# Optimization experiments

Measured on AMD Instinct MI355X. Metric: run time of the kernel, lower is better.

The kernel has to match this reference:

```python
import jax, jax.numpy as jnp
import numpy as np

N, E = 50000, 800000
IN, MID, OUT = 128, 256, 128
LN_EPS = 1e-5


def layer_norm(x, gamma, beta, eps=LN_EPS):
    mu = jnp.mean(x, axis=-1, keepdims=True)
    var = jnp.mean(jnp.square(x - mu), axis=-1, keepdims=True)
    return (x - mu) * jax.lax.rsqrt(var + eps) * gamma + beta


def gcn_conv(x, W, b, src, dst, norm, n):
    # x' = D^{-1/2}(A+I)D^{-1/2} X W + b  (self-loops already folded into src/dst/norm)
    h = x @ W                                  # [N, F_out]
    msg = h[src] * norm[:, None]               # [E+N, F_out] gather + scale
    out = jax.ops.segment_sum(msg, dst, num_segments=n)
    return out + b


def setup_inputs() -> dict:
    key = jax.random.key(0)
    ks = jax.random.split(key, 4)
    x = jax.random.normal(ks[0], (N, IN), dtype=jnp.float32)
    edge_index = jax.random.randint(ks[1], (2, E), 0, N, dtype=jnp.int32)
    W1 = jax.random.normal(ks[2], (IN, MID), dtype=jnp.float32) * (1.0 / np.sqrt(IN))
    b1 = jnp.zeros((MID,), jnp.float32)
    g1 = jnp.ones((IN,), jnp.float32)
    be1 = jnp.zeros((IN,), jnp.float32)
    W4 = jax.random.normal(ks[3], (MID, OUT), dtype=jnp.float32) * (1.0 / np.sqrt(MID))
    b4 = jnp.zeros((OUT,), jnp.float32)
    g4 = jnp.ones((MID,), jnp.float32)
    be4 = jnp.zeros((MID,), jnp.float32)
    return {"x": x, "W1": W1, "b1": b1, "g1": g1, "be1": be1,
            "W4": W4, "b4": b4, "g4": g4, "be4": be4,
            "edge_index": edge_index}


def reference(x, W1, b1, g1, be1, W4, b4, g4, be4, edge_index):
    n = x.shape[0]
    loop = jnp.arange(n, dtype=edge_index.dtype)
    src = jnp.concatenate([edge_index[0], loop])   # [E+N]
    dst = jnp.concatenate([edge_index[1], loop])   # [E+N]
    deg = jax.ops.segment_sum(jnp.ones_like(src, x.dtype), dst, num_segments=n)
    dinv = jax.lax.rsqrt(deg)                      # deg >= 1 thanks to self-loops
    norm = dinv[src] * dinv[dst]                   # [E+N]

    h = gcn_conv(layer_norm(x, g1, be1), W1, b1, src, dst, norm, n)
    h = jax.nn.gelu(h, approximate=False)          # torch F.gelu default = exact erf
    h = gcn_conv(layer_norm(h, g4, be4), W4, b4, src, dst, norm, n)
    return h
```

## Files before the change

kernel.cpp:

```cpp
#include <hip/hip_runtime.h>
#include <math.h>

#define N_NODES 50000
#define E_EDGES 800000

typedef __attribute__((ext_vector_type(4))) float f32x4;
typedef __attribute__((ext_vector_type(8))) short s16x8;

#define T1_OFF    0UL
#define A1H_OFF   12800000UL
#define A1L_OFF   25600000UL
#define T2B_OFF   38400000UL
#define WB1H_OFF  64000000UL
#define WB1L_OFF  64100096UL
#define WB4H_OFF  64200192UL
#define WB4L_OFF  64300288UL
#define DINV_OFF  64400384UL
#define HIST8_OFF 64600384UL
#define RP8_OFF   66200384UL
#define POSREL_OFF 67800448UL
#define CSRS_OFF  71000448UL
#define BSUM_OFF  74200448UL

__device__ __forceinline__ float lo16f(unsigned u) { return __uint_as_float(u << 16); }
__device__ __forceinline__ float hi16f(unsigned u) { return __uint_as_float(u & 0xffff0000u); }
__device__ __forceinline__ unsigned pack2bf(float a, float b) {
  unsigned ua = __float_as_uint(a); ua += 0x7fffu + ((ua >> 16) & 1u);
  unsigned ub = __float_as_uint(b); ub += 0x7fffu + ((ub >> 16) & 1u);
  return (ua >> 16) | (ub & 0xffff0000u);
}
__device__ __forceinline__ float gelu_f(float x) {
  return 0.5f * x * (1.f + erff(x * 0.70710678118654752f));
}

__global__ __launch_bounds__(256) void zero_hist8(int4* __restrict__ h) {
  int i = blockIdx.x * 256 + threadIdx.x;
  if (i < 100000) h[i] = make_int4(0, 0, 0, 0);
}

__global__ __launch_bounds__(256) void edge_pos(const int* __restrict__ dst,
                                                int* __restrict__ hist8,
                                                int* __restrict__ posrel) {
  int e = blockIdx.x * 256 + threadIdx.x;
  int d = dst[e];
  int seg = blockIdx.x & 7;
  int r = atomicAdd(&hist8[d * 8 + seg], 1);
  __builtin_nontemporal_store(r, posrel + e);
}

__global__ __launch_bounds__(1024) void scan_partial(const int* __restrict__ hist,
                                                     int* __restrict__ rp,
                                                     int* __restrict__ bsum, int n) {
  __shared__ int wsum[16];
  int tid = threadIdx.x, lane = tid & 63, wv = tid >> 6;
  int i = blockIdx.x * 1024 + tid;
  int v = (i < n) ? hist[i] : 0;
  int sc = v;
  #pragma unroll
  for (int m = 1; m < 64; m <<= 1) { int o = __shfl_up(sc, m); if (lane >= m) sc += o; }
  if (lane == 63) wsum[wv] = sc;
  __syncthreads();
  if (wv == 0) {
    int w = (lane < 16) ? wsum[lane] : 0;
    int swc = w;
    #pragma unroll
    for (int m = 1; m < 16; m <<= 1) { int o = __shfl_up(swc, m); if (lane >= m) swc += o; }
    if (lane < 16) wsum[lane] = swc - w;
    if (lane == 15) bsum[blockIdx.x] = swc;
  }
  __syncthreads();
  if (i < n) rp[i] = (sc - v) + wsum[wv];
}

__global__ __launch_bounds__(64) void scan_bsums(int* __restrict__ bsum, int nb) {
  int lane = threadIdx.x;
  int carry = 0;
  for (int base = 0; base < nb; base += 64) {
    int i = base + lane;
    int v = (i < nb) ? bsum[i] : 0;
    int sc = v;
    #pragma unroll
    for (int m = 1; m < 64; m <<= 1) { int o = __shfl_up(sc, m); if (lane >= m) sc += o; }
    if (i < nb) bsum[i] = carry + sc - v;
    carry += __shfl(sc, 63);
  }
  if (lane == 0) bsum[nb] = carry;
}

__global__ __launch_bounds__(1024) void scan_add(int* __restrict__ rp,
                                                 const int* __restrict__ bsum, int n) {
  int i = blockIdx.x * 1024 + threadIdx.x;
  if (i < n) rp[i] += bsum[blockIdx.x];
  if (i == 0) rp[n] = bsum[gridDim.x];
}

__global__ __launch_bounds__(256) void dinv_kernel(const int* __restrict__ hist8,
                                                   float* __restrict__ dinv, int n) {
  int i = blockIdx.x * 256 + threadIdx.x;
  if (i < n) {
    int4 a = *reinterpret_cast<const int4*>(hist8 + i * 8);
    int4 b = *reinterpret_cast<const int4*>(hist8 + i * 8 + 4);
    int deg = a.x + a.y + a.z + a.w + b.x + b.y + b.z + b.w;
    dinv[i] = rsqrtf((float)(deg + 1));
  }
}

__global__ __launch_bounds__(256) void fill2(const int* __restrict__ src,
                                             const int* __restrict__ dst,
                                             const int* __restrict__ rp8,
                                             const int* __restrict__ posrel,
                                             int* __restrict__ csr_src) {
  int e = blockIdx.x * 256 + threadIdx.x;
  int s = src[e], d = dst[e];
  int seg = blockIdx.x & 7;
  int pos = rp8[d * 8 + seg] + posrel[e];
  __builtin_nontemporal_store(s, csr_src + pos);
}

__global__ __launch_bounds__(256) void convW_split(const float* __restrict__ W,
                                                   unsigned* __restrict__ Wh,
                                                   unsigned* __restrict__ Wl, int K, int N) {
  int tid = blockIdx.x * 256 + threadIdx.x;
  if (tid >= (K * N) / 8) return;
  int c15 = tid & 15;
  int kg  = (tid >> 4) & 3;
  int KS  = K >> 5;
  int ks  = (tid >> 6) % KS;
  int nt  = (tid >> 6) / KS;
  int col = nt * 16 + c15;
  int k0  = ks * 32 + kg * 8;
  float w[8];
  #pragma unroll
  for (int j = 0; j < 8; ++j) w[j] = W[(size_t)(k0 + j) * N + col];
  uint4 h, l;
  h.x = pack2bf(w[0], w[1]); l.x = pack2bf(w[0] - lo16f(h.x), w[1] - hi16f(h.x));
  h.y = pack2bf(w[2], w[3]); l.y = pack2bf(w[2] - lo16f(h.y), w[3] - hi16f(h.y));
  h.z = pack2bf(w[4], w[5]); l.z = pack2bf(w[4] - lo16f(h.z), w[5] - hi16f(h.z));
  h.w = pack2bf(w[6], w[7]); l.w = pack2bf(w[6] - lo16f(h.w), w[7] - hi16f(h.w));
  *reinterpret_cast<uint4*>(Wh + (size_t)tid * 4) = h;
  *reinterpret_cast<uint4*>(Wl + (size_t)tid * 4) = l;
}

__global__ __launch_bounds__(256) void ln1_kernel(const float* __restrict__ x,
                                                  const float* __restrict__ g,
                                                  const float* __restrict__ be,
                                                  unsigned* __restrict__ T) {
  int lane = threadIdx.x & 63, wv = threadIdx.x >> 6;
  int row = blockIdx.x * 4 + wv;
  float2 v = *reinterpret_cast<const float2*>(x + (size_t)row * 128 + lane * 2);
  float s = v.x + v.y, sq = v.x * v.x + v.y * v.y;
  #pragma unroll
  for (int m = 1; m < 64; m <<= 1) { s += __shfl_xor(s, m); sq += __shfl_xor(sq, m); }
  float mu = s * (1.f / 128.f);
  float var = sq * (1.f / 128.f) - mu * mu;
  float rs = rsqrtf(var + 1e-5f);
  float2 gg = *reinterpret_cast<const float2*>(g + lane * 2);
  float2 bb = *reinterpret_cast<const float2*>(be + lane * 2);
  T[(size_t)row * 64 + lane] =
      pack2bf((v.x - mu) * rs * gg.x + bb.x, (v.y - mu) * rs * gg.y + bb.y);
}

template <int MODE>
__global__ __launch_bounds__(256) void agg128(const unsigned* __restrict__ T,
                                              const int* __restrict__ rp8,
                                              const int* __restrict__ csr_src,
                                              const float* __restrict__ dinv,
                                              const float* __restrict__ b,
                                              float* __restrict__ out,
                                              unsigned* __restrict__ outh,
                                              unsigned* __restrict__ outl) {
  int lane = threadIdx.x & 63, wv = threadIdx.x >> 6;
  int node = blockIdx.x * 4 + wv;
  float di = dinv[node], sn = di * di;
  unsigned us = T[(size_t)node * 64 + lane];
  float a0 = lo16f(us) * sn, a1 = hi16f(us) * sn;
  int e = rp8[node * 8], e1 = rp8[node * 8 + 8];
  for (; e + 3 < e1; e += 4) {
    int4 c = *reinterpret_cast<const int4*>(csr_src + e);
    unsigned u0 = T[(size_t)c.x * 64 + lane];
    unsigned u1 = T[(size_t)c.y * 64 + lane];
    unsigned u2 = T[(size_t)c.z * 64 + lane];
    unsigned u3 = T[(size_t)c.w * 64 + lane];
    float n0 = dinv[c.x] * di, n1 = dinv[c.y] * di;
    float n2 = dinv[c.z] * di, n3 = dinv[c.w] * di;
    a0 += lo16f(u0) * n0; a1 += hi16f(u0) * n0;
    a0 += lo16f(u1) * n1; a1 += hi16f(u1) * n1;
    a0 += lo16f(u2) * n2; a1 += hi16f(u2) * n2;
    a0 += lo16f(u3) * n3; a1 += hi16f(u3) * n3;
  }
  for (; e < e1; ++e) {
    int s = csr_src[e];
    unsigned u = T[(size_t)s * 64 + lane];
    float nr = dinv[s] * di;
    a0 += lo16f(u) * nr; a1 += hi16f(u) * nr;
  }
  if (MODE == 0) {
    unsigned h = pack2bf(a0, a1);
    float r0 = a0 - lo16f(h), r1 = a1 - hi16f(h);
    outh[(size_t)node * 64 + lane] = h;
    outl[(size_t)node * 64 + lane] = pack2bf(r0, r1);
  } else {
    float2 bb = *reinterpret_cast<const float2*>(b + lane * 2);
    *reinterpret_cast<float2*>(out + (size_t)node * 128 + lane * 2) =
        make_float2(a0 + bb.x, a1 + bb.y);
  }
}

__global__ __launch_bounds__(256) void gemm1_fused(const unsigned* __restrict__ Ah,
                                                   const unsigned* __restrict__ Al,
                                                   const unsigned* __restrict__ Wh,
                                                   const unsigned* __restrict__ Wl,
                                                   const float* __restrict__ b,
                                                   const float* __restrict__ g,
                                                   const float* __restrict__ be,
                                                   unsigned* __restrict__ T2b, int n) {
  __shared__ float st[32 * 260];
  int t = threadIdx.x, lane = t & 63, w = t >> 6;
  int kg = lane >> 4, c15 = lane & 15;
  int c0 = w * 64;
  int row0 = blockIdx.x * 32 + c15;
  int r0 = min(row0, n - 1);
  int r1 = min(row0 + 16, n - 1);
  const unsigned* ah0 = Ah + (size_t)r0 * 64 + kg * 4;
  const unsigned* al0 = Al + (size_t)r0 * 64 + kg * 4;
  const unsigned* ah1 = Ah + (size_t)r1 * 64 + kg * 4;
  const unsigned* al1 = Al + (size_t)r1 * 64 + kg * 4;
  f32x4 acc[2][4];
  #pragma unroll
  for (int rt = 0; rt < 2; ++rt)
    #pragma unroll
    for (int nf = 0; nf < 4; ++nf) acc[rt][nf] = (f32x4)(0.f);
  #pragma unroll
  for (int ks = 0; ks < 4; ++ks) {
    s16x8 bh[4], bl[4];
    #pragma unroll
    for (int nf = 0; nf < 4; ++nf) {
      int nt = (c0 >> 4) + nf;
      size_t bo = (size_t)(((nt * 4 + ks) * 4 + kg) * 16 + c15) * 4;
      bh[nf] = *reinterpret_cast<const s16x8*>(Wh + bo);
      bl[nf] = *reinterpret_cast<const s16x8*>(Wl + bo);
    }
    s16x8 a0h = *reinterpret_cast<const s16x8*>(ah0 + ks * 16);
    s16x8 a0l = *reinterpret_cast<const s16x8*>(al0 + ks * 16);
    s16x8 a1h = *reinterpret_cast<const s16x8*>(ah1 + ks * 16);
    s16x8 a1l = *reinterpret_cast<const s16x8*>(al1 + ks * 16);
    #pragma unroll
    for (int nf = 0; nf < 4; ++nf) {
      acc[0][nf] = __builtin_amdgcn_mfma_f32_16x16x32_bf16(a0h, bh[nf], acc[0][nf], 0, 0, 0);
      acc[0][nf] = __builtin_amdgcn_mfma_f32_16x16x32_bf16(a0l, bh[nf], acc[0][nf], 0, 0, 0);
      acc[0][nf] = __builtin_amdgcn_mfma_f32_16x16x32_bf16(a0h, bl[nf], acc[0][nf], 0, 0, 0);
      acc[1][nf] = __builtin_amdgcn_mfma_f32_16x16x32_bf16(a1h, bh[nf], acc[1][nf], 0, 0, 0);
      acc[1][nf] = __builtin_amdgcn_mfma_f32_16x16x32_bf16(a1l, bh[nf], acc[1][nf], 0, 0, 0);
      acc[1][nf] = __builtin_amdgcn_mfma_f32_16x16x32_bf16(a1h, bl[nf], acc[1][nf], 0, 0, 0);
    }
  }
  #pragma unroll
  for (int rt = 0; rt < 2; ++rt)
    #pragma unroll
    for (int nf = 0; nf < 4; ++nf) {
      int col = c0 + nf * 16 + c15;
      float bb = b[col];
      #pragma unroll
      for (int r = 0; r < 4; ++r) {
        int row = rt * 16 + kg * 4 + r;
        st[row * 260 + col] = gelu_f(acc[rt][nf][r] + bb);
      }
    }
  __syncthreads();
  float4 gg = *reinterpret_cast<const float4*>(g + lane * 4);
  float4 bb2 = *reinterpret_cast<const float4*>(be + lane * 4);
  #pragma unroll
  for (int rr = 0; rr < 8; ++rr) {
    int row = w * 8 + rr;
    float4 v = *reinterpret_cast<const float4*>(&st[row * 260 + lane * 4]);
    float s = v.x + v.y + v.z + v.w;
    float sq = v.x * v.x + v.y * v.y + v.z * v.z + v.w * v.w;
    #pragma unroll
    for (int m = 1; m < 64; m <<= 1) { s += __shfl_xor(s, m); sq += __shfl_xor(sq, m); }
    float mu = s * (1.f / 256.f);
    float var = sq * (1.f / 256.f) - mu * mu;
    float rs = rsqrtf(var + 1e-5f);
    int gr = blockIdx.x * 32 + row;
    if (gr < n) {
      uint2 p;
      p.x = pack2bf((v.x - mu) * rs * gg.x + bb2.x, (v.y - mu) * rs * gg.y + bb2.y);
      p.y = pack2bf((v.z - mu) * rs * gg.z + bb2.z, (v.w - mu) * rs * gg.w + bb2.w);
      *reinterpret_cast<uint2*>(T2b + (size_t)gr * 128 + lane * 2) = p;
    }
  }
}

__global__ __launch_bounds__(256) void gemm2_mfma(const unsigned* __restrict__ Ab,
                                                  const unsigned* __restrict__ Wh,
                                                  const unsigned* __restrict__ Wl,
                                                  unsigned* __restrict__ T2, int n) {
  __shared__ float st[32 * 132];
  int t = threadIdx.x, lane = t & 63, w = t >> 6;
  int kg = lane >> 4, c15 = lane & 15;
  int c0 = w * 32;
  int row0 = blockIdx.x * 32 + c15;
  int r0 = min(row0, n - 1);
  int r1 = min(row0 + 16, n - 1);
  const unsigned* ap0 = Ab + (size_t)r0 * 128 + kg * 4;
  const unsigned* ap1 = Ab + (size_t)r1 * 128 + kg * 4;
  f32x4 acc[2][2];
  #pragma unroll
  for (int rt = 0; rt < 2; ++rt) { acc[rt][0] = (f32x4)(0.f); acc[rt][1] = (f32x4)(0.f); }
  #pragma unroll
  for (int ks = 0; ks < 8; ++ks) {
    s16x8 bh[2], bl[2];
    #pragma unroll
    for (int nf = 0; nf < 2; ++nf) {
      int nt = (c0 >> 4) + nf;
      size_t bo = (size_t)(((nt * 8 + ks) * 4 + kg) * 16 + c15) * 4;
      bh[nf] = *reinterpret_cast<const s16x8*>(Wh + bo);
      bl[nf] = *reinterpret_cast<const s16x8*>(Wl + bo);
    }
    s16x8 a0 = *reinterpret_cast<const s16x8*>(ap0 + ks * 16);
    s16x8 a1 = *reinterpret_cast<const s16x8*>(ap1 + ks * 16);
    #pragma unroll
    for (int nf = 0; nf < 2; ++nf) {
      acc[0][nf] = __builtin_amdgcn_mfma_f32_16x16x32_bf16(a0, bh[nf], acc[0][nf], 0, 0, 0);
      acc[0][nf] = __builtin_amdgcn_mfma_f32_16x16x32_bf16(a0, bl[nf], acc[0][nf], 0, 0, 0);
      acc[1][nf] = __builtin_amdgcn_mfma_f32_16x16x32_bf16(a1, bh[nf], acc[1][nf], 0, 0, 0);
      acc[1][nf] = __builtin_amdgcn_mfma_f32_16x16x32_bf16(a1, bl[nf], acc[1][nf], 0, 0, 0);
    }
  }
  #pragma unroll
  for (int rt = 0; rt < 2; ++rt)
    #pragma unroll
    for (int nf = 0; nf < 2; ++nf) {
      int col = c0 + nf * 16 + c15;
      #pragma unroll
      for (int r = 0; r < 4; ++r) {
        int row = rt * 16 + kg * 4 + r;
        st[row * 132 + col] = acc[rt][nf][r];
      }
    }
  __syncthreads();
  #pragma unroll
  for (int rr = 0; rr < 8; ++rr) {
    int row = w * 8 + rr;
    int gr = blockIdx.x * 32 + row;
    if (gr < n) {
      float2 v = *reinterpret_cast<const float2*>(&st[row * 132 + lane * 2]);
      T2[(size_t)gr * 64 + lane] = pack2bf(v.x, v.y);
    }
  }
}

extern "C" void kernel_launch(void* const* d_in, const int* in_sizes, int n_in,
                              void* d_out, int out_size, void* d_ws, size_t ws_size,
                              hipStream_t stream) {
  (void)in_sizes; (void)n_in; (void)out_size; (void)ws_size;
  const float* x   = (const float*)d_in[0];
  const float* W1  = (const float*)d_in[1];
  const float* b1  = (const float*)d_in[2];
  const float* g1  = (const float*)d_in[3];
  const float* be1 = (const float*)d_in[4];
  const float* W4  = (const float*)d_in[5];
  const float* b4  = (const float*)d_in[6];
  const float* g4  = (const float*)d_in[7];
  const float* be4 = (const float*)d_in[8];
  const int*   ei  = (const int*)d_in[9];
  const int* src = ei;
  const int* dst = ei + E_EDGES;

  char* ws = (char*)d_ws;
  unsigned* T1    = (unsigned*)(ws + T1_OFF);
  unsigned* T2    = (unsigned*)(ws + T1_OFF);
  unsigned* A1h   = (unsigned*)(ws + A1H_OFF);
  unsigned* A1l   = (unsigned*)(ws + A1L_OFF);
  unsigned* T2b   = (unsigned*)(ws + T2B_OFF);
  unsigned* Wb1h  = (unsigned*)(ws + WB1H_OFF);
  unsigned* Wb1l  = (unsigned*)(ws + WB1L_OFF);
  unsigned* Wb4h  = (unsigned*)(ws + WB4H_OFF);
  unsigned* Wb4l  = (unsigned*)(ws + WB4L_OFF);
  float* dinv     = (float*)(ws + DINV_OFF);
  int*   hist8    = (int*)(ws + HIST8_OFF);
  int*   rp8      = (int*)(ws + RP8_OFF);
  int*   posrel   = (int*)(ws + POSREL_OFF);
  int*   csr_src  = (int*)(ws + CSRS_OFF);
  int*   bsum     = (int*)(ws + BSUM_OFF);
  float* outp     = (float*)d_out;

  const int NSEG = N_NODES * 8;
  int nblkE  = E_EDGES / 256;
  int nbScan = (NSEG + 1023) / 1024;
  int nblkG  = (N_NODES + 31) / 32;

  hipLaunchKernelGGL(zero_hist8, dim3(391), dim3(256), 0, stream, (int4*)hist8);
  hipLaunchKernelGGL(edge_pos, dim3(nblkE), dim3(256), 0, stream, dst, hist8, posrel);
  hipLaunchKernelGGL(dinv_kernel, dim3((N_NODES + 255) / 256), dim3(256), 0, stream,
                     hist8, dinv, N_NODES);
  hipLaunchKernelGGL(scan_partial, dim3(nbScan), dim3(1024), 0, stream, hist8, rp8, bsum, NSEG);
  hipLaunchKernelGGL(scan_bsums, dim3(1), dim3(64), 0, stream, bsum, nbScan);
  hipLaunchKernelGGL(scan_add, dim3(nbScan), dim3(1024), 0, stream, rp8, bsum, NSEG);
  hipLaunchKernelGGL(fill2, dim3(nblkE), dim3(256), 0, stream, src, dst, rp8, posrel, csr_src);
  hipLaunchKernelGGL(convW_split, dim3(16), dim3(256), 0, stream, W1, Wb1h, Wb1l, 128, 256);
  hipLaunchKernelGGL(convW_split, dim3(16), dim3(256), 0, stream, W4, Wb4h, Wb4l, 256, 128);

  hipLaunchKernelGGL(ln1_kernel, dim3(N_NODES / 4), dim3(256), 0, stream, x, g1, be1, T1);
  hipLaunchKernelGGL(agg128<0>, dim3(N_NODES / 4), dim3(256), 0, stream,
                     T1, rp8, csr_src, dinv, (const float*)nullptr,
                     (float*)nullptr, A1h, A1l);
  hipLaunchKernelGGL(gemm1_fused, dim3(nblkG), dim3(256), 0, stream,
                     A1h, A1l, Wb1h, Wb1l, b1, g4, be4, T2b, N_NODES);

  hipLaunchKernelGGL(gemm2_mfma, dim3(nblkG), dim3(256), 0, stream, T2b, Wb4h, Wb4l, T2, N_NODES);
  hipLaunchKernelGGL(agg128<2>, dim3(N_NODES / 4), dim3(256), 0, stream,
                     T2, rp8, csr_src, dinv, b4, outp,
                     (unsigned*)nullptr, (unsigned*)nullptr);
}
```

Baseline: 231.9 us.

## Compress CSR indices to 16-bit, pipeline aggregation gathers, fuse small setup kernels

Stores CSR source indices as unsigned short instead of int and restructures the aggregation loop into 8-wide batches that prefetch the next index batch and use two accumulator pairs. It also folds the degree-inverse computation into the scan kernel and merges the two weight-conversion launches into one. The goals are less index traffic, more gathers in flight, and fewer launches. Node ids go up to 50000, which fits in 16 bits, but this hard-codes that assumption about graph size.

```diff
diff --git a/kernel.cpp b/kernel.cpp
--- a/kernel.cpp
+++ b/kernel.cpp
@@ -50,11 +50,16 @@
 
 __global__ __launch_bounds__(1024) void scan_partial(const int* __restrict__ hist,
                                                      int* __restrict__ rp,
-                                                     int* __restrict__ bsum, int n) {
+                                                     int* __restrict__ bsum,
+                                                     float* __restrict__ dinv, int n) {
   __shared__ int wsum[16];
   int tid = threadIdx.x, lane = tid & 63, wv = tid >> 6;
   int i = blockIdx.x * 1024 + tid;
   int v = (i < n) ? hist[i] : 0;
+  int s8 = v;
+  #pragma unroll
+  for (int m = 1; m < 8; m <<= 1) s8 += __shfl_xor(s8, m);
+  if ((i & 7) == 0 && i < n) dinv[i >> 3] = rsqrtf((float)(s8 + 1));
   int sc = v;
   #pragma unroll
   for (int m = 1; m < 64; m <<= 1) { int o = __shfl_up(sc, m); if (lane >= m) sc += o; }
@@ -94,33 +99,22 @@
   if (i == 0) rp[n] = bsum[gridDim.x];
 }
 
-__global__ __launch_bounds__(256) void dinv_kernel(const int* __restrict__ hist8,
-                                                   float* __restrict__ dinv, int n) {
-  int i = blockIdx.x * 256 + threadIdx.x;
-  if (i < n) {
-    int4 a = *reinterpret_cast<const int4*>(hist8 + i * 8);
-    int4 b = *reinterpret_cast<const int4*>(hist8 + i * 8 + 4);
-    int deg = a.x + a.y + a.z + a.w + b.x + b.y + b.z + b.w;
-    dinv[i] = rsqrtf((float)(deg + 1));
-  }
-}
-
 __global__ __launch_bounds__(256) void fill2(const int* __restrict__ src,
                                              const int* __restrict__ dst,
                                              const int* __restrict__ rp8,
                                              const int* __restrict__ posrel,
-                                             int* __restrict__ csr_src) {
+                                             unsigned short* __restrict__ csr_src) {
   int e = blockIdx.x * 256 + threadIdx.x;
   int s = src[e], d = dst[e];
   int seg = blockIdx.x & 7;
   int pos = rp8[d * 8 + seg] + posrel[e];
-  __builtin_nontemporal_store(s, csr_src + pos);
-}
-
-__global__ __launch_bounds__(256) void convW_split(const float* __restrict__ W,
-                                                   unsigned* __restrict__ Wh,
-                                                   unsigned* __restrict__ Wl, int K, int N) {
-  int tid = blockIdx.x * 256 + threadIdx.x;
+  __builtin_nontemporal_store((unsigned short)s, csr_src + pos);
+}
+
+__device__ __forceinline__ void convW_body(const float* __restrict__ W,
+                                           unsigned* __restrict__ Wh,
+                                           unsigned* __restrict__ Wl,
+                                           int K, int N, int tid) {
   if (tid >= (K * N) / 8) return;
   int c15 = tid & 15;
   int kg  = (tid >> 4) & 3;
@@ -141,6 +135,17 @@
   *reinterpret_cast<uint4*>(Wl + (size_t)tid * 4) = l;
 }
 
+__global__ __launch_bounds__(256) void convW_both(const float* __restrict__ W1,
+                                                  const float* __restrict__ W4,
+                                                  unsigned* __restrict__ Wh1,
+                                                  unsigned* __restrict__ Wl1,
+                                                  unsigned* __restrict__ Wh4,
+                                                  unsigned* __restrict__ Wl4) {
+  int b = blockIdx.x;
+  if (b < 16) convW_body(W1, Wh1, Wl1, 128, 256, b * 256 + threadIdx.x);
+  else        convW_body(W4, Wh4, Wl4, 256, 128, (b - 16) * 256 + threadIdx.x);
+}
+
 __global__ __launch_bounds__(256) void ln1_kernel(const float* __restrict__ x,
                                                   const float* __restrict__ g,
                                                   const float* __restrict__ be,
@@ -163,7 +168,7 @@
 template <int MODE>
 __global__ __launch_bounds__(256) void agg128(const unsigned* __restrict__ T,
                                               const int* __restrict__ rp8,
-                                              const int* __restrict__ csr_src,
+                                              const unsigned short* __restrict__ csr,
                                               const float* __restrict__ dinv,
                                               const float* __restrict__ b,
                                               float* __restrict__ out,
@@ -174,26 +179,44 @@
   float di = dinv[node], sn = di * di;
   unsigned us = T[(size_t)node * 64 + lane];
   float a0 = lo16f(us) * sn, a1 = hi16f(us) * sn;
+  float b0 = 0.f, b1 = 0.f;
   int e = rp8[node * 8], e1 = rp8[node * 8 + 8];
-  for (; e + 3 < e1; e += 4) {
-    int4 c = *reinterpret_cast<const int4*>(csr_src + e);
-    unsigned u0 = T[(size_t)c.x * 64 + lane];
-    unsigned u1 = T[(size_t)c.y * 64 + lane];
-    unsigned u2 = T[(size_t)c.z * 64 + lane];
-    unsigned u3 = T[(size_t)c.w * 64 + lane];
-    float n0 = dinv[c.x] * di, n1 = dinv[c.y] * di;
-    float n2 = dinv[c.z] * di, n3 = dinv[c.w] * di;
-    a0 += lo16f(u0) * n0; a1 += hi16f(u0) * n0;
-    a0 += lo16f(u1) * n1; a1 += hi16f(u1) * n1;
-    a0 += lo16f(u2) * n2; a1 += hi16f(u2) * n2;
-    a0 += lo16f(u3) * n3; a1 += hi16f(u3) * n3;
+  if (e + 7 < e1) {
+    int sA[8];
+    #pragma unroll
+    for (int j = 0; j < 8; ++j) sA[j] = csr[e + j];
+    for (;;) {
+      unsigned u[8];
+      float nn[8];
+      #pragma unroll
+      for (int j = 0; j < 8; ++j) u[j] = T[(size_t)sA[j] * 64 + lane];
+      #pragma unroll
+      for (int j = 0; j < 8; ++j) nn[j] = dinv[sA[j]];
+      e += 8;
+      bool more = (e + 7 < e1);
+      int sB[8];
+      if (more) {
+        #pragma unroll
+        for (int j = 0; j < 8; ++j) sB[j] = csr[e + j];
+      }
+      #pragma unroll
+      for (int j = 0; j < 8; ++j) {
+        float nr = nn[j] * di;
+        if (j & 1) { b0 += lo16f(u[j]) * nr; b1 += hi16f(u[j]) * nr; }
+        else       { a0 += lo16f(u[j]) * nr; a1 += hi16f(u[j]) * nr; }
+      }
+      if (!more) break;
+      #pragma unroll
+      for (int j = 0; j < 8; ++j) sA[j] = sB[j];
+    }
   }
   for (; e < e1; ++e) {
-    int s = csr_src[e];
+    int s = csr[e];
     unsigned u = T[(size_t)s * 64 + lane];
     float nr = dinv[s] * di;
     a0 += lo16f(u) * nr; a1 += hi16f(u) * nr;
   }
+  a0 += b0; a1 += b1;
   if (MODE == 0) {
     unsigned h = pack2bf(a0, a1);
     float r0 = a0 - lo16f(h), r1 = a1 - hi16f(h);
@@ -380,7 +403,7 @@
   int*   hist8    = (int*)(ws + HIST8_OFF);
   int*   rp8      = (int*)(ws + RP8_OFF);
   int*   posrel   = (int*)(ws + POSREL_OFF);
-  int*   csr_src  = (int*)(ws + CSRS_OFF);
+  unsigned short* csr_src = (unsigned short*)(ws + CSRS_OFF);
   int*   bsum     = (int*)(ws + BSUM_OFF);
   float* outp     = (float*)d_out;
 
@@ -391,14 +414,13 @@
 
   hipLaunchKernelGGL(zero_hist8, dim3(391), dim3(256), 0, stream, (int4*)hist8);
   hipLaunchKernelGGL(edge_pos, dim3(nblkE), dim3(256), 0, stream, dst, hist8, posrel);
-  hipLaunchKernelGGL(dinv_kernel, dim3((N_NODES + 255) / 256), dim3(256), 0, stream,
-                     hist8, dinv, N_NODES);
-  hipLaunchKernelGGL(scan_partial, dim3(nbScan), dim3(1024), 0, stream, hist8, rp8, bsum, NSEG);
+  hipLaunchKernelGGL(scan_partial, dim3(nbScan), dim3(1024), 0, stream,
+                     hist8, rp8, bsum, dinv, NSEG);
   hipLaunchKernelGGL(scan_bsums, dim3(1), dim3(64), 0, stream, bsum, nbScan);
   hipLaunchKernelGGL(scan_add, dim3(nbScan), dim3(1024), 0, stream, rp8, bsum, NSEG);
   hipLaunchKernelGGL(fill2, dim3(nblkE), dim3(256), 0, stream, src, dst, rp8, posrel, csr_src);
-  hipLaunchKernelGGL(convW_split, dim3(16), dim3(256), 0, stream, W1, Wb1h, Wb1l, 128, 256);
-  hipLaunchKernelGGL(convW_split, dim3(16), dim3(256), 0, stream, W4, Wb4h, Wb4l, 256, 128);
+  hipLaunchKernelGGL(convW_both, dim3(32), dim3(256), 0, stream,
+                     W1, W4, Wb1h, Wb1l, Wb4h, Wb4l);
 
   hipLaunchKernelGGL(ln1_kernel, dim3(N_NODES / 4), dim3(256), 0, stream, x, g1, be1, T1);
   hipLaunchKernelGGL(agg128<0>, dim3(N_NODES / 4), dim3(256), 0, stream,
```

Result: no change. 233.8 us (+0.8%).
